# Optimization experiments

Hardware: AMD Instinct MI355X
Metric: run time of the kernel (lower is better)

The kernel has to match this reference:

```python
import jax, jax.numpy as jnp
import numpy as np

B, N, P, K, D = 8, 2048, 64, 32, 384
DEPTH, DI, DS, DCONV, DTR, NC = 12, 768, 16, 4, 24, 40
BN_EPS = 1e-5


def _spread_bits(v):
    v = v & 1023
    v = (v | (v << 16)) & 50331903
    v = (v | (v << 8)) & 50393103
    v = (v | (v << 4)) & 51130563
    v = (v | (v << 2)) & 153391689
    return v


def _zkey(x, y, z):
    return _spread_bits(x) | (_spread_bits(y) << 1) | (_spread_bits(z) << 2)


def _sfc_order(xyz, trans):
    lo = xyz.min(0, keepdims=True)
    hi = xyz.max(0, keepdims=True)
    q = jnp.clip(((xyz - lo) / (hi - lo + 1e-6) * 1023.0).astype(jnp.int32), 0, 1023)
    if trans:
        keys = _zkey(q[:, 2], q[:, 1], q[:, 0])
    else:
        keys = _zkey(q[:, 0], q[:, 1], q[:, 2])
    return jnp.argsort(keys)


def _ln(x, g, b):
    m = x.mean(-1, keepdims=True)
    v = jnp.var(x, axis=-1, keepdims=True)
    return (x - m) / jnp.sqrt(v + 1e-5) * g + b


def _bn_eval(x, g, b):
    # BatchNorm in eval mode, running_mean=0 / running_var=1
    return x * (g / np.float32(np.sqrt(1.0 + BN_EPS))) + b


def _patch_embed_one(xyz, w1, b1, g1, be1, w2, b2, g2, be2, w3, b3, g3, be3):
    # xyz: (N,3)
    cidx = (jnp.arange(P) * (N / P)).astype(jnp.int32)
    centers = xyz[cidx]                                      # (P,3)
    d2 = ((centers[:, None, :] - xyz[None, :, :]) ** 2).sum(-1)  # (P,N)
    _, knn = jax.lax.top_k(-d2, K)                           # (P,K) smallest dists
    nx = xyz[knn] - centers[:, None, :]                      # (P,K,3)
    h = jax.nn.gelu(_bn_eval(nx @ w1.T + b1, g1, be1), approximate=False)   # (P,K,64)
    h = jax.nn.gelu(_bn_eval(h @ w2.T + b2, g2, be2), approximate=False)    # (P,K,128)
    h = _bn_eval(h @ w3.T + b3, g3, be3)                     # (P,K,384)
    return h.max(1), centers


def _mamba(x, in_w, conv_w, conv_b, xp_w, dt_w, dt_b, Alog, Dp, out_w):
    # x: (B,L,D)
    Bsz, L, _ = x.shape
    xz = x @ in_w.T                                          # (B,L,2*DI)
    xc, z = xz[..., :DI], xz[..., DI:]
    xpad = jnp.pad(xc, ((0, 0), (DCONV - 1, 0), (0, 0)))
    xc = sum(xpad[:, j:j + L, :] * conv_w[:, j] for j in range(DCONV)) + conv_b
    xc = jax.nn.silu(xc)
    x_dbl = xc @ xp_w.T                                      # (B,L,DTR+2*DS)
    dt = x_dbl[..., :DTR]
    Bm = x_dbl[..., DTR:DTR + DS]
    Cm = x_dbl[..., DTR + DS:]
    delta = jax.nn.softplus(dt @ dt_w.T + dt_b)              # (B,L,DI)
    A = -jnp.exp(Alog)                                       # (DI,DS)

    def step(h, inp):
        d_t, B_t, C_t, u_t = inp                             # (B,DI),(B,DS),(B,DS),(B,DI)
        h = h * jnp.exp(d_t[..., None] * A) + (d_t * u_t)[..., None] * B_t[:, None, :]
        return h, jnp.einsum('bds,bs->bd', h, C_t)

    h0 = jnp.zeros((Bsz, DI, DS), x.dtype)
    inps = (delta.transpose(1, 0, 2), Bm.transpose(1, 0, 2),
            Cm.transpose(1, 0, 2), xc.transpose(1, 0, 2))
    _, ys = jax.lax.scan(step, h0, inps)                     # (L,B,DI)
    y = ys.transpose(1, 0, 2) + Dp * xc
    y = y * jax.nn.silu(z)
    return y @ out_w.T


def setup_inputs() -> dict:
    key = jax.random.key(0)
    ks = iter(jax.random.split(key, 64))
    nrm = lambda *s: jax.random.normal(next(ks), s, jnp.float32) * 0.02
    inp = {
        'data': jax.random.normal(next(ks), (B, N, 3), jnp.float32),
        'pe_w1': nrm(64, 3), 'pe_b1': jnp.zeros(64), 'pe_g1': jnp.ones(64), 'pe_be1': jnp.zeros(64),
        'pe_w2': nrm(128, 64), 'pe_b2': jnp.zeros(128), 'pe_g2': jnp.ones(128), 'pe_be2': jnp.zeros(128),
        'pe_w3': nrm(D, 128), 'pe_b3': jnp.zeros(D), 'pe_g3': jnp.ones(D), 'pe_be3': jnp.zeros(D),
        'oi_h_scale': jnp.ones(D), 'oi_h_shift': jnp.zeros(D),
        'oi_th_scale': jnp.ones(D), 'oi_th_shift': jnp.zeros(D),
        'pos_embed': nrm(1, P, D),
        'blk_ln_g': jnp.ones((DEPTH, D)), 'blk_ln_b': jnp.zeros((DEPTH, D)),
        'blk_in_w': nrm(DEPTH, 2 * DI, D),
        'blk_conv_w': nrm(DEPTH, DI, DCONV), 'blk_conv_b': jnp.zeros((DEPTH, DI)),
        'blk_xp_w': nrm(DEPTH, DTR + 2 * DS, DI),
        'blk_dt_w': nrm(DEPTH, DI, DTR), 'blk_dt_b': jnp.full((DEPTH, DI), -4.0),
        'blk_Alog': jnp.tile(jnp.log(jnp.arange(1, DS + 1, dtype=jnp.float32)), (DEPTH, DI, 1)),
        'blk_D': jnp.ones((DEPTH, DI)),
        'blk_out_w': nrm(DEPTH, D, DI),
        'norm_g': jnp.ones(D), 'norm_b': jnp.zeros(D),
        'mlp_w1': nrm(256, D), 'mlp_b1': jnp.zeros(256),
        'mlp_w2': nrm(64, 256), 'mlp_b2': jnp.zeros(64),
        'mlp_w3': nrm(NC, 64), 'mlp_b3': jnp.zeros(NC),
    }
    return inp


def reference(data, pe_w1, pe_b1, pe_g1, pe_be1, pe_w2, pe_b2, pe_g2, pe_be2,
              pe_w3, pe_b3, pe_g3, pe_be3, oi_h_scale, oi_h_shift, oi_th_scale,
              oi_th_shift, pos_embed, blk_ln_g, blk_ln_b, blk_in_w, blk_conv_w,
              blk_conv_b, blk_xp_w, blk_dt_w, blk_dt_b, blk_Alog, blk_D,
              blk_out_w, norm_g, norm_b, mlp_w1, mlp_b1, mlp_w2, mlp_b2,
              mlp_w3, mlp_b3):
    xyz = data[:, :, :3]
    tokens, centers = jax.vmap(
        _patch_embed_one, in_axes=(0,) + (None,) * 12)(
        xyz, pe_w1, pe_b1, pe_g1, pe_be1, pe_w2, pe_b2, pe_g2, pe_be2,
        pe_w3, pe_b3, pe_g3, pe_be3)                         # (B,P,D),(B,P,3)
    order_h = jax.vmap(lambda c: _sfc_order(c, False))(centers)
    order_th = jax.vmap(lambda c: _sfc_order(c, True))(centers)
    th = jnp.take_along_axis(tokens, order_h[:, :, None], axis=1) * oi_h_scale + oi_h_shift
    tth = jnp.take_along_axis(tokens, order_th[:, :, None], axis=1) * oi_th_scale + oi_th_shift
    t = jnp.concatenate([th + pos_embed, tth + pos_embed], axis=1)  # (B,2P,D)
    for i in range(DEPTH):
        t = t + _mamba(_ln(t, blk_ln_g[i], blk_ln_b[i]),
                       blk_in_w[i], blk_conv_w[i], blk_conv_b[i], blk_xp_w[i],
                       blk_dt_w[i], blk_dt_b[i], blk_Alog[i], blk_D[i], blk_out_w[i])
    t = _ln(t, norm_g, norm_b)
    x = t.mean(1)
    x = jax.nn.relu(x @ mlp_w1.T + mlp_b1)
    x = jax.nn.relu(x @ mlp_w2.T + mlp_b2)
    return x @ mlp_w3.T + mlp_b3
```

## Files before the change

kernel.cpp:

```cpp
#include <hip/hip_runtime.h>
#include <math.h>

#define BB 8
#define NN 2048
#define PP 64
#define KK 32
#define DD 384
#define DEPTH 12
#define DI 768
#define DS 16
#define DCONV 4
#define DTR 24
#define NC 40
#define LL 128
#define XROW (DTR + 2 * DS)
#define NR (BB * LL)
#define XPARTS 12

using bf16x8 = __attribute__((ext_vector_type(8))) short;
using floatx4 = __attribute__((ext_vector_type(4))) float;

__device__ __forceinline__ float gelu_exact(float x) {
    return 0.5f * x * (1.0f + erff(x * 0.70710678118654752440f));
}
__device__ __forceinline__ float siluf(float x) {
    return x / (1.0f + expf(-x));
}
__device__ __forceinline__ unsigned short f2bf(float f) {
    unsigned u = __float_as_uint(f);
    u += 0x7fffu + ((u >> 16) & 1u);
    return (unsigned short)(u >> 16);
}
__device__ __forceinline__ float bf2f(short s) {
    return __uint_as_float(((unsigned)(unsigned short)s) << 16);
}
__device__ __forceinline__ unsigned spread_bits(unsigned v) {
    v &= 1023u;
    v = (v | (v << 16)) & 50331903u;
    v = (v | (v << 8)) & 50393103u;
    v = (v | (v << 4)) & 51130563u;
    v = (v | (v << 2)) & 153391689u;
    return v;
}

__global__ void k_cvt(const float* __restrict__ in_w, const float* __restrict__ out_w,
                      const float* __restrict__ pe_w3, const float* __restrict__ xp,
                      unsigned short* __restrict__ inwbf, unsigned short* __restrict__ owbf,
                      unsigned short* __restrict__ w3bf, unsigned short* __restrict__ xpbf)
{
    int idx = blockIdx.x * 256 + threadIdx.x;
    const int n1 = DEPTH * 2 * DI * DD;
    const int n2 = DEPTH * DD * DI;
    const int n3 = DD * 128;
    const int n4 = DEPTH * 64 * DI;
    if (idx < n1) { inwbf[idx] = f2bf(in_w[idx]); return; }
    idx -= n1;
    if (idx < n2) { owbf[idx] = f2bf(out_w[idx]); return; }
    idx -= n2;
    if (idx < n3) { w3bf[idx] = f2bf(pe_w3[idx]); return; }
    idx -= n3;
    if (idx < n4) {
        int i = idx / (64 * DI);
        int rem = idx - i * 64 * DI;
        int n = rem / DI, k = rem % DI;
        float v = (n < XROW) ? xp[(size_t)i * XROW * DI + (size_t)n * DI + k] : 0.f;
        xpbf[idx] = f2bf(v);
    }
}

__global__ __launch_bounds__(256) void k_knn(const float* __restrict__ data,
                                             int* __restrict__ knn_out,
                                             float* __restrict__ centers)
{
    const int bp = blockIdx.x;
    const int b = bp >> 6, p = bp & 63;
    const int tid = threadIdx.x;
    const int lane = tid & 63, wid = tid >> 6;
    const float* X = data + (size_t)b * NN * 3;

    const float cx = X[p * 32 * 3 + 0];
    const float cy = X[p * 32 * 3 + 1];
    const float cz = X[p * 32 * 3 + 2];
    if (tid == 0) {
        centers[(b * PP + p) * 3 + 0] = cx;
        centers[(b * PP + p) * 3 + 1] = cy;
        centers[(b * PP + p) * 3 + 2] = cz;
    }

    unsigned long long pk[8];
#pragma unroll
    for (int q = 0; q < 8; q++) {
        int i = tid + 256 * q;
        float dx = cx - X[i * 3 + 0];
        float dy = cy - X[i * 3 + 1];
        float dz = cz - X[i * 3 + 2];
        float d2 = dx * dx + dy * dy + dz * dz;
        pk[q] = ((unsigned long long)__float_as_uint(d2) << 32) | (unsigned)i;
    }

    __shared__ unsigned long long wred[4];
    __shared__ int klist[KK];
    for (int k = 0; k < KK; k++) {
        unsigned long long m = pk[0];
#pragma unroll
        for (int q = 1; q < 8; q++) m = pk[q] < m ? pk[q] : m;
#pragma unroll
        for (int off = 32; off; off >>= 1) {
            unsigned long long o = __shfl_xor(m, off);
            m = o < m ? o : m;
        }
        if (lane == 0) wred[wid] = m;
        __syncthreads();
        unsigned long long g = wred[0];
#pragma unroll
        for (int w = 1; w < 4; w++) g = wred[w] < g ? wred[w] : g;
#pragma unroll
        for (int q = 0; q < 8; q++)
            if (pk[q] == g) pk[q] = ~0ull;
        if (tid == 0) klist[k] = (int)(g & 0xffffffffu);
        __syncthreads();
    }
    if (tid < KK) knn_out[bp * KK + tid] = klist[tid];
}

__global__ __launch_bounds__(256) void k_pe_mlp(
    const float* __restrict__ data, const int* __restrict__ knn_in,
    const float* __restrict__ w1, const float* __restrict__ b1,
    const float* __restrict__ g1, const float* __restrict__ be1,
    const float* __restrict__ w2, const float* __restrict__ b2,
    const float* __restrict__ g2, const float* __restrict__ be2,
    const unsigned short* __restrict__ w3bf, const float* __restrict__ b3,
    const float* __restrict__ g3, const float* __restrict__ be3,
    float* __restrict__ tokens)
{
    const int bp = blockIdx.x;
    const int b = bp >> 6, p = bp & 63;
    const int tid = threadIdx.x;
    const float* X = data + (size_t)b * NN * 3;
    const float inv_den = 0.99999500003749968752f;

    __shared__ float nxs[KK * 3];
    __shared__ float h1s[KK * 64];
    __shared__ short h2b[KK * 136];

    const float cx = X[p * 32 * 3 + 0];
    const float cy = X[p * 32 * 3 + 1];
    const float cz = X[p * 32 * 3 + 2];
    if (tid < KK) {
        int q = knn_in[bp * KK + tid];
        nxs[tid * 3 + 0] = X[q * 3 + 0] - cx;
        nxs[tid * 3 + 1] = X[q * 3 + 1] - cy;
        nxs[tid * 3 + 2] = X[q * 3 + 2] - cz;
    }
    __syncthreads();

    for (int e = tid; e < KK * 64; e += 256) {
        int j = e >> 6, c = e & 63;
        float v = nxs[j * 3 + 0] * w1[c * 3 + 0] + nxs[j * 3 + 1] * w1[c * 3 + 1] +
                  nxs[j * 3 + 2] * w1[c * 3 + 2] + b1[c];
        v = v * (g1[c] * inv_den) + be1[c];
        h1s[j * 64 + c] = gelu_exact(v);
    }
    __syncthreads();

    for (int e = tid; e < KK * 128; e += 256) {
        int j = e >> 7, c = e & 127;
        const float4* wr = (const float4*)(w2 + (size_t)c * 64);
        const float4* hr = (const float4*)(h1s + j * 64);
        float acc = 0.f;
#pragma unroll
        for (int q = 0; q < 16; q++) {
            float4 wv = wr[q], hv = hr[q];
            acc += hv.x * wv.x + hv.y * wv.y + hv.z * wv.z + hv.w * wv.w;
        }
        float v = (acc + b2[c]) * (g2[c] * inv_den) + be2[c];
        h2b[j * 136 + c] = (short)f2bf(gelu_exact(v));
    }
    __syncthreads();

    const int wave = tid >> 6, lane = tid & 63;
    const int quad = lane >> 4, r = lane & 15;
    floatx4 acc3[2][6] = {};
#pragma unroll
    for (int ks = 0; ks < 4; ks++) {
        const int k0 = ks * 32;
        bf16x8 af[2];
        af[0] = *(const bf16x8*)(h2b + (size_t)r * 136 + quad * 8 + k0);
        af[1] = *(const bf16x8*)(h2b + (size_t)(16 + r) * 136 + quad * 8 + k0);
        bf16x8 bfv[6];
#pragma unroll
        for (int nj = 0; nj < 6; nj++) {
            int n = wave * 96 + nj * 16 + r;
            bfv[nj] = *(const bf16x8*)(w3bf + (size_t)n * 128 + quad * 8 + k0);
        }
#pragma unroll
        for (int mi = 0; mi < 2; mi++)
#pragma unroll
            for (int nj = 0; nj < 6; nj++)
                acc3[mi][nj] = __builtin_amdgcn_mfma_f32_16x16x32_bf16(af[mi], bfv[nj], acc3[mi][nj], 0, 0, 0);
    }
#pragma unroll
    for (int nj = 0; nj < 6; nj++) {
        int col = wave * 96 + nj * 16 + r;
        float sc = g3[col] * inv_den;
        float offc = b3[col] * sc + be3[col];
        float m = -3.4e38f;
#pragma unroll
        for (int mi = 0; mi < 2; mi++)
#pragma unroll
            for (int r2 = 0; r2 < 4; r2++)
                m = fmaxf(m, acc3[mi][nj][r2] * sc + offc);
        m = fmaxf(m, __shfl_xor(m, 16));
        m = fmaxf(m, __shfl_xor(m, 32));
        if (quad == 0) tokens[(size_t)bp * DD + col] = m;
    }
}

__global__ __launch_bounds__(64) void k_sfc(const float* __restrict__ centers,
                                            int* __restrict__ order_h,
                                            int* __restrict__ order_th)
{
    const int b = blockIdx.x;
    const int tid = threadIdx.x;
    float cc[3];
    cc[0] = centers[(b * PP + tid) * 3 + 0];
    cc[1] = centers[(b * PP + tid) * 3 + 1];
    cc[2] = centers[(b * PP + tid) * 3 + 2];

    __shared__ float csh[PP][3];
    __shared__ float slo[3], shi[3];
    csh[tid][0] = cc[0]; csh[tid][1] = cc[1]; csh[tid][2] = cc[2];
    __syncthreads();
    if (tid == 0) {
        for (int k = 0; k < 3; k++) {
            float lo = csh[0][k], hi = csh[0][k];
            for (int j = 1; j < PP; j++) { lo = fminf(lo, csh[j][k]); hi = fmaxf(hi, csh[j][k]); }
            slo[k] = lo; shi[k] = hi;
        }
    }
    __syncthreads();

    int q[3];
    for (int k = 0; k < 3; k++) {
        float t = (cc[k] - slo[k]) / (shi[k] - slo[k] + 1e-6f) * 1023.0f;
        int qi = (int)t;
        qi = qi < 0 ? 0 : (qi > 1023 ? 1023 : qi);
        q[k] = qi;
    }
    unsigned kh = spread_bits((unsigned)q[0]) | (spread_bits((unsigned)q[1]) << 1) |
                  (spread_bits((unsigned)q[2]) << 2);
    unsigned kt = spread_bits((unsigned)q[2]) | (spread_bits((unsigned)q[1]) << 1) |
                  (spread_bits((unsigned)q[0]) << 2);

    __shared__ unsigned khs[PP], kts[PP];
    khs[tid] = kh; kts[tid] = kt;
    __syncthreads();
    int rh = 0, rt = 0;
    for (int j = 0; j < PP; j++) {
        unsigned a = khs[j];
        rh += (a < kh) || (a == kh && j < tid);
        unsigned c = kts[j];
        rt += (c < kt) || (c == kt && j < tid);
    }
    order_h[b * PP + rh] = tid;
    order_th[b * PP + rt] = tid;
}

__global__ void k_build_t(const float* __restrict__ tokens,
                          const int* __restrict__ order_h, const int* __restrict__ order_th,
                          const float* __restrict__ hs, const float* __restrict__ hb,
                          const float* __restrict__ ts, const float* __restrict__ tb,
                          const float* __restrict__ pos, float* __restrict__ t)
{
    int idx = blockIdx.x * blockDim.x + threadIdx.x;
    if (idx >= BB * LL * DD) return;
    int d = idx % DD;
    int l = (idx / DD) % LL;
    int b = idx / (DD * LL);
    float v;
    if (l < PP) {
        int src = order_h[b * PP + l];
        v = tokens[((size_t)b * PP + src) * DD + d] * hs[d] + hb[d] + pos[l * DD + d];
    } else {
        int ll2 = l - PP;
        int src = order_th[b * PP + ll2];
        v = tokens[((size_t)b * PP + src) * DD + d] * ts[d] + tb[d] + pos[ll2 * DD + d];
    }
    t[idx] = v;
}

__global__ __launch_bounds__(256) void k_stats(const float* __restrict__ t,
                                               const float* __restrict__ g,
                                               const float* __restrict__ gb,
                                               unsigned short* __restrict__ tbf)
{
    const int tid = threadIdx.x;
    const int wid = tid >> 6, lane = tid & 63;
    const int row = blockIdx.x * 4 + wid;
    const size_t base = (size_t)row * DD;
    float v[6];
    float s = 0.f, q = 0.f;
#pragma unroll
    for (int j = 0; j < 6; j++) {
        v[j] = t[base + lane + 64 * j];
        s += v[j]; q += v[j] * v[j];
    }
#pragma unroll
    for (int off = 32; off; off >>= 1) { s += __shfl_xor(s, off); q += __shfl_xor(q, off); }
    float mean = s * (1.0f / DD);
    float var = q * (1.0f / DD) - mean * mean;
    float inv = 1.0f / sqrtf(var + 1e-5f);
#pragma unroll
    for (int j = 0; j < 6; j++) {
        int i = lane + 64 * j;
        tbf[base + i] = f2bf((v[j] - mean) * inv * g[i] + gb[i]);
    }
}

__global__ __launch_bounds__(256) void k_mfma_xz(
    const unsigned short* __restrict__ tbf,
    const unsigned short* __restrict__ inwbf,
    const float* __restrict__ cw, const float* __restrict__ cb,
    const unsigned short* __restrict__ xpbf,
    unsigned short* __restrict__ xcbf, unsigned short* __restrict__ zsbf,
    float* __restrict__ parts_x)
{
    __shared__ short ct[128][72];
    const int tid = threadIdx.x;
    const int wave = tid >> 6, lane = tid & 63;
    const int quad = lane >> 4, r = lane & 15;
    const int wm = wave >> 1, wn = wave & 1;
    const int b = blockIdx.y;
    const int n0 = blockIdx.x * 64;
    const int m0 = b * 128 + wm * 64;

    floatx4 acc[4][2] = {};
    const unsigned short* Ab = tbf + (size_t)(m0 + r) * DD + quad * 8;
    const unsigned short* Bb = inwbf + (size_t)(n0 + wn * 32 + r) * DD + quad * 8;
    for (int k0 = 0; k0 < DD; k0 += 32) {
        bf16x8 af[4], bfv[2];
#pragma unroll
        for (int i = 0; i < 4; i++)
            af[i] = *(const bf16x8*)(Ab + (size_t)(i * 16) * DD + k0);
#pragma unroll
        for (int j = 0; j < 2; j++)
            bfv[j] = *(const bf16x8*)(Bb + (size_t)(j * 16) * DD + k0);
#pragma unroll
        for (int i = 0; i < 4; i++)
#pragma unroll
            for (int j = 0; j < 2; j++)
                acc[i][j] = __builtin_amdgcn_mfma_f32_16x16x32_bf16(af[i], bfv[j], acc[i][j], 0, 0, 0);
    }

#pragma unroll
    for (int i = 0; i < 4; i++)
#pragma unroll
        for (int r2 = 0; r2 < 4; r2++) {
            short* cp = &ct[wm * 64 + i * 16 + quad * 4 + r2][wn * 32 + r];
#pragma unroll
            for (int j = 0; j < 2; j++)
                cp[j * 16] = (short)f2bf(acc[i][j][r2]);
        }
    __syncthreads();

    const int l0 = (tid >> 3) * 4;
    const int c0 = (tid & 7) * 8;
    if (n0 < DI) {
        float cwv[8][4], cbv[8];
#pragma unroll
        for (int q = 0; q < 8; q++) {
            *(float4*)cwv[q] = *(const float4*)(cw + (size_t)(n0 + c0 + q) * 4);
            cbv[q] = cb[n0 + c0 + q];
        }
        unsigned short ov[4][8];
#pragma unroll
        for (int dl = 0; dl < 4; dl++) {
            const int l = l0 + dl;
            float u[8];
#pragma unroll
            for (int q = 0; q < 8; q++) u[q] = cbv[q];
#pragma unroll
            for (int j = 0; j < DCONV; j++) {
                int lt = l - (DCONV - 1) + j;
                if (lt >= 0) {
                    bf16x8 x = *(const bf16x8*)&ct[lt][c0];
#pragma unroll
                    for (int q = 0; q < 8; q++) u[q] += bf2f(x[q]) * cwv[q][j];
                }
            }
#pragma unroll
            for (int q = 0; q < 8; q++) ov[dl][q] = f2bf(siluf(u[q]));
        }
        __syncthreads();
#pragma unroll
        for (int dl = 0; dl < 4; dl++) {
            const int l = l0 + dl;
            *(bf16x8*)&ct[l][c0] = *(bf16x8*)ov[dl];
            *(bf16x8*)(xcbf + (size_t)(b * LL + l) * DI + n0 + c0) = *(bf16x8*)ov[dl];
        }
        __syncthreads();

        const int zi = blockIdx.x;
        floatx4 acc2[2][4] = {};
#pragma unroll
        for (int k0 = 0; k0 < 64; k0 += 32) {
            bf16x8 af2[2], bfv2[4];
#pragma unroll
            for (int i = 0; i < 2; i++)
                af2[i] = *(const bf16x8*)&ct[wave * 32 + i * 16 + r][k0 + quad * 8];
#pragma unroll
            for (int nj = 0; nj < 4; nj++)
                bfv2[nj] = *(const bf16x8*)(xpbf + (size_t)(nj * 16 + r) * DI + n0 + k0 + quad * 8);
#pragma unroll
            for (int i = 0; i < 2; i++)
#pragma unroll
                for (int nj = 0; nj < 4; nj++)
                    acc2[i][nj] = __builtin_amdgcn_mfma_f32_16x16x32_bf16(af2[i], bfv2[nj], acc2[i][nj], 0, 0, 0);
        }
        float* out = parts_x + (size_t)zi * NR * XROW;
#pragma unroll
        for (int i = 0; i < 2; i++)
#pragma unroll
            for (int nj = 0; nj < 4; nj++) {
                int col = nj * 16 + r;
                if (col < XROW) {
#pragma unroll
                    for (int r2 = 0; r2 < 4; r2++) {
                        int row = b * LL + wave * 32 + i * 16 + quad * 4 + r2;
                        out[(size_t)row * XROW + col] = acc2[i][nj][r2];
                    }
                }
            }
    } else {
        const int nz = n0 - DI;
#pragma unroll
        for (int dl = 0; dl < 4; dl++) {
            const int l = l0 + dl;
            bf16x8 x = *(const bf16x8*)&ct[l][c0];
            unsigned short o[8];
#pragma unroll
            for (int q = 0; q < 8; q++) o[q] = f2bf(siluf(bf2f(x[q])));
            *(bf16x8*)(zsbf + (size_t)(b * LL + l) * DI + nz + c0) = *(bf16x8*)o;
        }
    }
}

__global__ void k_xred(const float* __restrict__ parts, float* __restrict__ xdbl)
{
    int i = blockIdx.x * 256 + threadIdx.x;
    if (i >= NR * XROW) return;
    float s = 0.f;
#pragma unroll
    for (int z = 0; z < XPARTS; z++) s += parts[(size_t)z * NR * XROW + i];
    xdbl[i] = s;
}

__global__ __launch_bounds__(128) void k_scan(
    const float* __restrict__ xdbl,
    const unsigned short* __restrict__ xcbf, const unsigned short* __restrict__ zsbf,
    const float* __restrict__ dtw, const float* __restrict__ dtb,
    const float* __restrict__ Alog, const float* __restrict__ Dp,
    unsigned short* __restrict__ ybf)
{
    const int tid = threadIdx.x;
    const int b = blockIdx.x / DI;
    const int d = blockIdx.x % DI;

    __shared__ float da[LL][17];
    __shared__ float Bsh[LL][17];
    __shared__ float Csh[LL][17];
    __shared__ float dus[LL];
    __shared__ float us[LL];
    __shared__ float zs[LL];
    __shared__ float ApL[DS][9];
    __shared__ float HlL[DS][9];
    __shared__ float hst[DS][9];

    {
        const int t = tid;
        const size_t row = (size_t)b * LL + t;
        const float* xd = xdbl + row * XROW;
        const float* w = dtw + d * DTR;
        float acc = dtb[d];
#pragma unroll
        for (int k = 0; k < DTR; k++) acc += xd[k] * w[k];
        float delta = fmaxf(acc, 0.f) + log1pf(__expf(-fabsf(acc)));
        float u = bf2f((short)xcbf[row * DI + d]);
        dus[t] = delta * u;
        us[t] = u;
        zs[t] = bf2f((short)zsbf[row * DI + d]);
#pragma unroll
        for (int s = 0; s < DS; s++) {
            da[t][s] = __expf(delta * (-__expf(Alog[d * DS + s])));
            Bsh[t][s] = xd[DTR + s];
            Csh[t][s] = xd[DTR + DS + s];
        }
    }
    __syncthreads();

    const int s = tid & 15;
    const int c = tid >> 4;

    {
        float h = 0.f, Ap = 1.f;
#pragma unroll
        for (int q = 0; q < 16; q++) {
            int t = c * 16 + q;
            float a = da[t][s];
            h = h * a + dus[t] * Bsh[t][s];
            Ap *= a;
        }
        ApL[s][c] = Ap;
        HlL[s][c] = h;
    }
    __syncthreads();
    if (tid < DS) {
        float hs = 0.f;
#pragma unroll
        for (int cc = 0; cc < 8; cc++) {
            hst[tid][cc] = hs;
            hs = ApL[tid][cc] * hs + HlL[tid][cc];
        }
    }
    __syncthreads();

    {
        const float Dd = Dp[d];
        float h = hst[s][c];
        unsigned short* yc = ybf + ((size_t)b * LL + c * 16) * DI + d;
#pragma unroll
        for (int q = 0; q < 16; q++) {
            int t = c * 16 + q;
            float a = da[t][s];
            h = h * a + dus[t] * Bsh[t][s];
            float p = h * Csh[t][s];
            p += __shfl_xor(p, 1, 16);
            p += __shfl_xor(p, 2, 16);
            p += __shfl_xor(p, 4, 16);
            p += __shfl_xor(p, 8, 16);
            if (s == 0) yc[(size_t)q * DI] = f2bf((p + Dd * us[t]) * zs[t]);
        }
    }
}

__global__ __launch_bounds__(256) void k_mfma_op(
    const unsigned short* __restrict__ ybf,
    const unsigned short* __restrict__ owbf,
    float* __restrict__ t)
{
    const int tid = threadIdx.x;
    const int wave = tid >> 6, lane = tid & 63;
    const int quad = lane >> 4, r = lane & 15;
    const int wr2 = wave >> 1, wc = wave & 1;
    const int n0 = blockIdx.x * 64 + wc * 32;
    const int m0 = blockIdx.y * 32 + wr2 * 16;

    floatx4 acc[2] = {};
    const unsigned short* Ab = ybf + (size_t)(m0 + r) * DI + quad * 8;
    const unsigned short* Bb = owbf + (size_t)(n0 + r) * DI + quad * 8;
    for (int k0 = 0; k0 < DI; k0 += 32) {
        bf16x8 af = *(const bf16x8*)(Ab + k0);
        bf16x8 b0 = *(const bf16x8*)(Bb + k0);
        bf16x8 b1 = *(const bf16x8*)(Bb + (size_t)16 * DI + k0);
        acc[0] = __builtin_amdgcn_mfma_f32_16x16x32_bf16(af, b0, acc[0], 0, 0, 0);
        acc[1] = __builtin_amdgcn_mfma_f32_16x16x32_bf16(af, b1, acc[1], 0, 0, 0);
    }

#pragma unroll
    for (int j = 0; j < 2; j++) {
        int col = n0 + j * 16 + r;
#pragma unroll
        for (int r2 = 0; r2 < 4; r2++) {
            int row = m0 + quad * 4 + r2;
            float* tp = t + (size_t)row * DD + col;
            *tp += acc[j][r2];
        }
    }
}

__global__ __launch_bounds__(256) void k_lnpool(const float* __restrict__ t,
                                                const float* __restrict__ ng,
                                                const float* __restrict__ nb,
                                                float* __restrict__ pparts)
{
    const int b = blockIdx.y, chunk = blockIdx.x;
    const int tid = threadIdx.x;
    const int wave = tid >> 6, lane = tid & 63;
    __shared__ float pw[4][DD];

    for (int c = lane; c < DD; c += 64) pw[wave][c] = 0.f;
    __syncthreads();

    for (int rr = 0; rr < 4; rr++) {
        const int row = b * LL + chunk * 16 + wave * 4 + rr;
        const float* xr = t + (size_t)row * DD;
        float v[6];
        float s = 0.f, q = 0.f;
#pragma unroll
        for (int j = 0; j < 6; j++) { v[j] = xr[lane + 64 * j]; s += v[j]; q += v[j] * v[j]; }
#pragma unroll
        for (int off = 32; off; off >>= 1) { s += __shfl_xor(s, off); q += __shfl_xor(q, off); }
        float mean = s * (1.0f / DD);
        float var = q * (1.0f / DD) - mean * mean;
        float inv = 1.0f / sqrtf(var + 1e-5f);
#pragma unroll
        for (int j = 0; j < 6; j++) {
            int c = lane + 64 * j;
            pw[wave][c] += (v[j] - mean) * inv * ng[c] + nb[c];
        }
    }
    __syncthreads();
    float* out = pparts + ((size_t)b * 8 + chunk) * DD;
    for (int c = tid; c < DD; c += 256)
        out[c] = pw[0][c] + pw[1][c] + pw[2][c] + pw[3][c];
}

__global__ __launch_bounds__(256) void k_mlp(const float* __restrict__ pparts,
    const float* __restrict__ w1, const float* __restrict__ b1,
    const float* __restrict__ w2, const float* __restrict__ b2,
    const float* __restrict__ w3, const float* __restrict__ b3,
    float* __restrict__ out)
{
    const int b = blockIdx.x, tid = threadIdx.x;
    __shared__ float pl[DD];
    __shared__ float h1[256];
    __shared__ float h2[64];
    for (int c = tid; c < DD; c += 256) {
        const float* pp = pparts + (size_t)b * 8 * DD + c;
        float s = 0.f;
#pragma unroll
        for (int z = 0; z < 8; z++) s += pp[z * DD];
        pl[c] = s * (1.0f / LL);
    }
    __syncthreads();

    {
        float acc = b1[tid];
        const float* wr = w1 + (size_t)tid * DD;
        for (int k = 0; k < DD; k++) acc += pl[k] * wr[k];
        h1[tid] = fmaxf(acc, 0.f);
    }
    __syncthreads();
    if (tid < 64) {
        float acc = b2[tid];
        const float* wr = w2 + (size_t)tid * 256;
        for (int k = 0; k < 256; k++) acc += h1[k] * wr[k];
        h2[tid] = fmaxf(acc, 0.f);
    }
    __syncthreads();
    if (tid < NC) {
        float acc = b3[tid];
        const float* wr = w3 + (size_t)tid * 64;
        for (int k = 0; k < 64; k++) acc += h2[k] * wr[k];
        out[b * NC + tid] = acc;
    }
}

extern "C" void kernel_launch(void* const* d_in, const int* in_sizes, int n_in,
                              void* d_out, int out_size, void* d_ws, size_t ws_size,
                              hipStream_t stream)
{
    const float* data      = (const float*)d_in[0];
    const float* pe_w1     = (const float*)d_in[1];
    const float* pe_b1     = (const float*)d_in[2];
    const float* pe_g1     = (const float*)d_in[3];
    const float* pe_be1    = (const float*)d_in[4];
    const float* pe_w2     = (const float*)d_in[5];
    const float* pe_b2     = (const float*)d_in[6];
    const float* pe_g2     = (const float*)d_in[7];
    const float* pe_be2    = (const float*)d_in[8];
    const float* pe_w3     = (const float*)d_in[9];
    const float* pe_b3     = (const float*)d_in[10];
    const float* pe_g3     = (const float*)d_in[11];
    const float* pe_be3    = (const float*)d_in[12];
    const float* oi_h_scale  = (const float*)d_in[13];
    const float* oi_h_shift  = (const float*)d_in[14];
    const float* oi_th_scale = (const float*)d_in[15];
    const float* oi_th_shift = (const float*)d_in[16];
    const float* pos_embed = (const float*)d_in[17];
    const float* blk_ln_g  = (const float*)d_in[18];
    const float* blk_ln_b  = (const float*)d_in[19];
    const float* blk_in_w  = (const float*)d_in[20];
    const float* blk_conv_w = (const float*)d_in[21];
    const float* blk_conv_b = (const float*)d_in[22];
    const float* blk_xp_w  = (const float*)d_in[23];
    const float* blk_dt_w  = (const float*)d_in[24];
    const float* blk_dt_b  = (const float*)d_in[25];
    const float* blk_Alog  = (const float*)d_in[26];
    const float* blk_D     = (const float*)d_in[27];
    const float* blk_out_w = (const float*)d_in[28];
    const float* norm_g    = (const float*)d_in[29];
    const float* norm_b    = (const float*)d_in[30];
    const float* mlp_w1    = (const float*)d_in[31];
    const float* mlp_b1    = (const float*)d_in[32];
    const float* mlp_w2    = (const float*)d_in[33];
    const float* mlp_b2    = (const float*)d_in[34];
    const float* mlp_w3    = (const float*)d_in[35];
    const float* mlp_b3    = (const float*)d_in[36];

    float* ws = (float*)d_ws;
    size_t off = 0;
    auto alloc = [&](size_t n) { float* p = ws + off; off += (n + 63) & ~(size_t)63; return p; };
    float* tokens  = alloc((size_t)BB * PP * DD);
    float* centers = alloc((size_t)BB * PP * 3);
    int*   order_h = (int*)alloc((size_t)BB * PP);
    int*   order_th= (int*)alloc((size_t)BB * PP);
    int*   knn_idx = (int*)alloc((size_t)BB * PP * KK);
    float* t    = alloc((size_t)NR * DD);
    float* xdbl = alloc((size_t)NR * XROW);
    float* parts_x = alloc((size_t)XPARTS * NR * XROW);
    float* pparts  = alloc((size_t)BB * 8 * DD);
    unsigned short* tbf   = (unsigned short*)alloc((size_t)NR * DD / 2);
    unsigned short* xcbf  = (unsigned short*)alloc((size_t)NR * DI / 2);
    unsigned short* zsbf  = (unsigned short*)alloc((size_t)NR * DI / 2);
    unsigned short* ybf   = (unsigned short*)alloc((size_t)NR * DI / 2);
    unsigned short* inwbf = (unsigned short*)alloc((size_t)DEPTH * 2 * DI * DD / 2);
    unsigned short* owbf  = (unsigned short*)alloc((size_t)DEPTH * DD * DI / 2);
    unsigned short* xpbf  = (unsigned short*)alloc((size_t)DEPTH * 64 * DI / 2);
    unsigned short* w3bf  = (unsigned short*)alloc((size_t)DD * 128 / 2);

    {
        const int total = DEPTH * 2 * DI * DD + DEPTH * DD * DI + DD * 128 + DEPTH * 64 * DI;
        k_cvt<<<(total + 255) / 256, 256, 0, stream>>>(
            blk_in_w, blk_out_w, pe_w3, blk_xp_w, inwbf, owbf, w3bf, xpbf);
    }

    k_knn<<<BB * PP, 256, 0, stream>>>(data, knn_idx, centers);
    k_pe_mlp<<<BB * PP, 256, 0, stream>>>(data, knn_idx,
        pe_w1, pe_b1, pe_g1, pe_be1, pe_w2, pe_b2, pe_g2, pe_be2,
        w3bf, pe_b3, pe_g3, pe_be3, tokens);
    k_sfc<<<BB, 64, 0, stream>>>(centers, order_h, order_th);
    {
        int nt = BB * LL * DD;
        k_build_t<<<(nt + 255) / 256, 256, 0, stream>>>(tokens, order_h, order_th,
            oi_h_scale, oi_h_shift, oi_th_scale, oi_th_shift, pos_embed, t);
    }

    for (int i = 0; i < DEPTH; i++) {
        const float* ln_g = blk_ln_g + i * DD;
        const float* ln_b = blk_ln_b + i * DD;
        const float* cw   = blk_conv_w + (size_t)i * DI * DCONV;
        const float* cb   = blk_conv_b + (size_t)i * DI;
        const float* dtw  = blk_dt_w + (size_t)i * DI * DTR;
        const float* dtb  = blk_dt_b + (size_t)i * DI;
        const float* Al   = blk_Alog + (size_t)i * DI * DS;
        const float* Dpp  = blk_D + (size_t)i * DI;
        const unsigned short* inw = inwbf + (size_t)i * 2 * DI * DD;
        const unsigned short* ow  = owbf + (size_t)i * DD * DI;
        const unsigned short* xpb = xpbf + (size_t)i * 64 * DI;

        k_stats<<<NR / 4, 256, 0, stream>>>(t, ln_g, ln_b, tbf);
        k_mfma_xz<<<dim3(24, BB), 256, 0, stream>>>(
            tbf, inw, cw, cb, xpb, xcbf, zsbf, parts_x);
        k_xred<<<(NR * XROW + 255) / 256, 256, 0, stream>>>(parts_x, xdbl);
        k_scan<<<BB * DI, 128, 0, stream>>>(xdbl, xcbf, zsbf, dtw, dtb, Al, Dpp, ybf);
        k_mfma_op<<<dim3(DD / 64, NR / 32), 256, 0, stream>>>(ybf, ow, t);
    }

    k_lnpool<<<dim3(8, BB), 256, 0, stream>>>(t, norm_g, norm_b, pparts);
    k_mlp<<<BB, 256, 0, stream>>>(pparts, mlp_w1, mlp_b1, mlp_w2, mlp_b2, mlp_w3, mlp_b3,
                                  (float*)d_out);
}
```

Baseline: 1.055 ms.

## Fuse kNN with patch MLP, SFC with token build, and atomically reduce x_proj

kNN selection moves into the patch-embedding kernel, and SFC ordering merges with token building, which removes launches and global round-trips. The per-layer partial-sum buffer plus its reduction kernel give way to atomic adds into xdbl, which the stats kernel now zeroes. k_cvt is vectorised to four elements per thread. The scan kernel computes decay terms on the fly and keeps per-step values in registers instead of large shared arrays. Atomics make the summation order nondeterministic and add contention, and the register arrays raise register pressure in the scan.

```diff
diff --git a/kernel.cpp b/kernel.cpp
--- a/kernel.cpp
+++ b/kernel.cpp
@@ -15,7 +15,6 @@
 #define LL 128
 #define XROW (DTR + 2 * DS)
 #define NR (BB * LL)
-#define XPARTS 12
 
 using bf16x8 = __attribute__((ext_vector_type(8))) short;
 using floatx4 = __attribute__((ext_vector_type(4))) float;
@@ -48,35 +47,68 @@
                       unsigned short* __restrict__ inwbf, unsigned short* __restrict__ owbf,
                       unsigned short* __restrict__ w3bf, unsigned short* __restrict__ xpbf)
 {
-    int idx = blockIdx.x * 256 + threadIdx.x;
+    int idx = (blockIdx.x * 256 + threadIdx.x) * 4;
     const int n1 = DEPTH * 2 * DI * DD;
     const int n2 = DEPTH * DD * DI;
     const int n3 = DD * 128;
     const int n4 = DEPTH * 64 * DI;
-    if (idx < n1) { inwbf[idx] = f2bf(in_w[idx]); return; }
+    if (idx < n1) {
+        float4 v = *(const float4*)(in_w + idx);
+        ushort4 o; o.x = f2bf(v.x); o.y = f2bf(v.y); o.z = f2bf(v.z); o.w = f2bf(v.w);
+        *(ushort4*)(inwbf + idx) = o;
+        return;
+    }
     idx -= n1;
-    if (idx < n2) { owbf[idx] = f2bf(out_w[idx]); return; }
+    if (idx < n2) {
+        float4 v = *(const float4*)(out_w + idx);
+        ushort4 o; o.x = f2bf(v.x); o.y = f2bf(v.y); o.z = f2bf(v.z); o.w = f2bf(v.w);
+        *(ushort4*)(owbf + idx) = o;
+        return;
+    }
     idx -= n2;
-    if (idx < n3) { w3bf[idx] = f2bf(pe_w3[idx]); return; }
+    if (idx < n3) {
+        float4 v = *(const float4*)(pe_w3 + idx);
+        ushort4 o; o.x = f2bf(v.x); o.y = f2bf(v.y); o.z = f2bf(v.z); o.w = f2bf(v.w);
+        *(ushort4*)(w3bf + idx) = o;
+        return;
+    }
     idx -= n3;
     if (idx < n4) {
         int i = idx / (64 * DI);
         int rem = idx - i * 64 * DI;
         int n = rem / DI, k = rem % DI;
-        float v = (n < XROW) ? xp[(size_t)i * XROW * DI + (size_t)n * DI + k] : 0.f;
-        xpbf[idx] = f2bf(v);
-    }
-}
-
-__global__ __launch_bounds__(256) void k_knn(const float* __restrict__ data,
-                                             int* __restrict__ knn_out,
-                                             float* __restrict__ centers)
+        ushort4 o;
+        if (n < XROW) {
+            float4 v = *(const float4*)(xp + (size_t)i * XROW * DI + (size_t)n * DI + k);
+            o.x = f2bf(v.x); o.y = f2bf(v.y); o.z = f2bf(v.z); o.w = f2bf(v.w);
+        } else {
+            o.x = o.y = o.z = o.w = 0;
+        }
+        *(ushort4*)(xpbf + (size_t)i * 64 * DI + (size_t)n * DI + k) = o;
+    }
+}
+
+__global__ __launch_bounds__(256) void k_patch(
+    const float* __restrict__ data,
+    const float* __restrict__ w1, const float* __restrict__ b1,
+    const float* __restrict__ g1, const float* __restrict__ be1,
+    const float* __restrict__ w2, const float* __restrict__ b2,
+    const float* __restrict__ g2, const float* __restrict__ be2,
+    const unsigned short* __restrict__ w3bf, const float* __restrict__ b3,
+    const float* __restrict__ g3, const float* __restrict__ be3,
+    float* __restrict__ tokens, float* __restrict__ centers)
 {
     const int bp = blockIdx.x;
     const int b = bp >> 6, p = bp & 63;
     const int tid = threadIdx.x;
-    const int lane = tid & 63, wid = tid >> 6;
     const float* X = data + (size_t)b * NN * 3;
+    const float inv_den = 0.99999500003749968752f;
+
+    __shared__ unsigned long long wred[4];
+    __shared__ int klist[KK];
+    __shared__ float nxs[KK * 3];
+    __shared__ float h1s[KK * 64];
+    __shared__ short h2b[KK * 136];
 
     const float cx = X[p * 32 * 3 + 0];
     const float cy = X[p * 32 * 3 + 1];
@@ -87,67 +119,42 @@
         centers[(b * PP + p) * 3 + 2] = cz;
     }
 
-    unsigned long long pk[8];
-#pragma unroll
-    for (int q = 0; q < 8; q++) {
-        int i = tid + 256 * q;
-        float dx = cx - X[i * 3 + 0];
-        float dy = cy - X[i * 3 + 1];
-        float dz = cz - X[i * 3 + 2];
-        float d2 = dx * dx + dy * dy + dz * dz;
-        pk[q] = ((unsigned long long)__float_as_uint(d2) << 32) | (unsigned)i;
-    }
-
-    __shared__ unsigned long long wred[4];
-    __shared__ int klist[KK];
-    for (int k = 0; k < KK; k++) {
-        unsigned long long m = pk[0];
-#pragma unroll
-        for (int q = 1; q < 8; q++) m = pk[q] < m ? pk[q] : m;
-#pragma unroll
-        for (int off = 32; off; off >>= 1) {
-            unsigned long long o = __shfl_xor(m, off);
-            m = o < m ? o : m;
-        }
-        if (lane == 0) wred[wid] = m;
-        __syncthreads();
-        unsigned long long g = wred[0];
-#pragma unroll
-        for (int w = 1; w < 4; w++) g = wred[w] < g ? wred[w] : g;
-#pragma unroll
-        for (int q = 0; q < 8; q++)
-            if (pk[q] == g) pk[q] = ~0ull;
-        if (tid == 0) klist[k] = (int)(g & 0xffffffffu);
-        __syncthreads();
-    }
-    if (tid < KK) knn_out[bp * KK + tid] = klist[tid];
-}
-
-__global__ __launch_bounds__(256) void k_pe_mlp(
-    const float* __restrict__ data, const int* __restrict__ knn_in,
-    const float* __restrict__ w1, const float* __restrict__ b1,
-    const float* __restrict__ g1, const float* __restrict__ be1,
-    const float* __restrict__ w2, const float* __restrict__ b2,
-    const float* __restrict__ g2, const float* __restrict__ be2,
-    const unsigned short* __restrict__ w3bf, const float* __restrict__ b3,
-    const float* __restrict__ g3, const float* __restrict__ be3,
-    float* __restrict__ tokens)
-{
-    const int bp = blockIdx.x;
-    const int b = bp >> 6, p = bp & 63;
-    const int tid = threadIdx.x;
-    const float* X = data + (size_t)b * NN * 3;
-    const float inv_den = 0.99999500003749968752f;
-
-    __shared__ float nxs[KK * 3];
-    __shared__ float h1s[KK * 64];
-    __shared__ short h2b[KK * 136];
-
-    const float cx = X[p * 32 * 3 + 0];
-    const float cy = X[p * 32 * 3 + 1];
-    const float cz = X[p * 32 * 3 + 2];
+    {
+        const int lane = tid & 63, wid = tid >> 6;
+        unsigned long long pk[8];
+#pragma unroll
+        for (int q = 0; q < 8; q++) {
+            int i = tid + 256 * q;
+            float dx = cx - X[i * 3 + 0];
+            float dy = cy - X[i * 3 + 1];
+            float dz = cz - X[i * 3 + 2];
+            float d2 = dx * dx + dy * dy + dz * dz;
+            pk[q] = ((unsigned long long)__float_as_uint(d2) << 32) | (unsigned)i;
+        }
+        for (int k = 0; k < KK; k++) {
+            unsigned long long m = pk[0];
+#pragma unroll
+            for (int q = 1; q < 8; q++) m = pk[q] < m ? pk[q] : m;
+#pragma unroll
+            for (int off = 32; off; off >>= 1) {
+                unsigned long long o = __shfl_xor(m, off);
+                m = o < m ? o : m;
+            }
+            if (lane == 0) wred[wid] = m;
+            __syncthreads();
+            unsigned long long g = wred[0];
+#pragma unroll
+            for (int w = 1; w < 4; w++) g = wred[w] < g ? wred[w] : g;
+#pragma unroll
+            for (int q = 0; q < 8; q++)
+                if (pk[q] == g) pk[q] = ~0ull;
+            if (tid == 0) klist[k] = (int)(g & 0xffffffffu);
+            __syncthreads();
+        }
+    }
+
     if (tid < KK) {
-        int q = knn_in[bp * KK + tid];
+        int q = klist[tid];
         nxs[tid * 3 + 0] = X[q * 3 + 0] - cx;
         nxs[tid * 3 + 1] = X[q * 3 + 1] - cy;
         nxs[tid * 3 + 2] = X[q * 3 + 2] - cz;
@@ -216,20 +223,25 @@
     }
 }
 
-__global__ __launch_bounds__(64) void k_sfc(const float* __restrict__ centers,
-                                            int* __restrict__ order_h,
-                                            int* __restrict__ order_th)
-{
-    const int b = blockIdx.x;
+__global__ __launch_bounds__(256) void k_sfc_build(
+    const float* __restrict__ centers, const float* __restrict__ tokens,
+    const float* __restrict__ hs, const float* __restrict__ hb,
+    const float* __restrict__ ts2, const float* __restrict__ tb2,
+    const float* __restrict__ pos, float* __restrict__ tout)
+{
+    const int b = blockIdx.y, part = blockIdx.x;
     const int tid = threadIdx.x;
-    float cc[3];
-    cc[0] = centers[(b * PP + tid) * 3 + 0];
-    cc[1] = centers[(b * PP + tid) * 3 + 1];
-    cc[2] = centers[(b * PP + tid) * 3 + 2];
 
     __shared__ float csh[PP][3];
     __shared__ float slo[3], shi[3];
-    csh[tid][0] = cc[0]; csh[tid][1] = cc[1]; csh[tid][2] = cc[2];
+    __shared__ unsigned khs[PP], kts[PP];
+    __shared__ int oh[PP], ot[PP];
+
+    if (tid < PP) {
+        csh[tid][0] = centers[(b * PP + tid) * 3 + 0];
+        csh[tid][1] = centers[(b * PP + tid) * 3 + 1];
+        csh[tid][2] = centers[(b * PP + tid) * 3 + 2];
+    }
     __syncthreads();
     if (tid == 0) {
         for (int k = 0; k < 3; k++) {
@@ -239,62 +251,63 @@
         }
     }
     __syncthreads();
-
-    int q[3];
-    for (int k = 0; k < 3; k++) {
-        float t = (cc[k] - slo[k]) / (shi[k] - slo[k] + 1e-6f) * 1023.0f;
-        int qi = (int)t;
-        qi = qi < 0 ? 0 : (qi > 1023 ? 1023 : qi);
-        q[k] = qi;
-    }
-    unsigned kh = spread_bits((unsigned)q[0]) | (spread_bits((unsigned)q[1]) << 1) |
-                  (spread_bits((unsigned)q[2]) << 2);
-    unsigned kt = spread_bits((unsigned)q[2]) | (spread_bits((unsigned)q[1]) << 1) |
-                  (spread_bits((unsigned)q[0]) << 2);
-
-    __shared__ unsigned khs[PP], kts[PP];
-    khs[tid] = kh; kts[tid] = kt;
-    __syncthreads();
-    int rh = 0, rt = 0;
-    for (int j = 0; j < PP; j++) {
-        unsigned a = khs[j];
-        rh += (a < kh) || (a == kh && j < tid);
-        unsigned c = kts[j];
-        rt += (c < kt) || (c == kt && j < tid);
-    }
-    order_h[b * PP + rh] = tid;
-    order_th[b * PP + rt] = tid;
-}
-
-__global__ void k_build_t(const float* __restrict__ tokens,
-                          const int* __restrict__ order_h, const int* __restrict__ order_th,
-                          const float* __restrict__ hs, const float* __restrict__ hb,
-                          const float* __restrict__ ts, const float* __restrict__ tb,
-                          const float* __restrict__ pos, float* __restrict__ t)
-{
-    int idx = blockIdx.x * blockDim.x + threadIdx.x;
-    if (idx >= BB * LL * DD) return;
-    int d = idx % DD;
-    int l = (idx / DD) % LL;
-    int b = idx / (DD * LL);
-    float v;
-    if (l < PP) {
-        int src = order_h[b * PP + l];
-        v = tokens[((size_t)b * PP + src) * DD + d] * hs[d] + hb[d] + pos[l * DD + d];
-    } else {
-        int ll2 = l - PP;
-        int src = order_th[b * PP + ll2];
-        v = tokens[((size_t)b * PP + src) * DD + d] * ts[d] + tb[d] + pos[ll2 * DD + d];
-    }
-    t[idx] = v;
+    if (tid < PP) {
+        int q[3];
+        for (int k = 0; k < 3; k++) {
+            float t = (csh[tid][k] - slo[k]) / (shi[k] - slo[k] + 1e-6f) * 1023.0f;
+            int qi = (int)t;
+            qi = qi < 0 ? 0 : (qi > 1023 ? 1023 : qi);
+            q[k] = qi;
+        }
+        khs[tid] = spread_bits((unsigned)q[0]) | (spread_bits((unsigned)q[1]) << 1) |
+                   (spread_bits((unsigned)q[2]) << 2);
+        kts[tid] = spread_bits((unsigned)q[2]) | (spread_bits((unsigned)q[1]) << 1) |
+                   (spread_bits((unsigned)q[0]) << 2);
+    }
+    __syncthreads();
+    if (tid < PP) {
+        unsigned kh = khs[tid], kt = kts[tid];
+        int rh = 0, rt = 0;
+        for (int j = 0; j < PP; j++) {
+            unsigned a = khs[j];
+            rh += (a < kh) || (a == kh && j < tid);
+            unsigned c = kts[j];
+            rt += (c < kt) || (c == kt && j < tid);
+        }
+        oh[rh] = tid;
+        ot[rt] = tid;
+    }
+    __syncthreads();
+
+    const int base = part * (LL * DD / 24);
+    for (int e = tid; e < LL * DD / 24; e += 256) {
+        int idx = base + e;
+        int d = idx % DD;
+        int l = idx / DD;
+        float v;
+        if (l < PP) {
+            int src = oh[l];
+            v = tokens[((size_t)b * PP + src) * DD + d] * hs[d] + hb[d] + pos[l * DD + d];
+        } else {
+            int l2 = l - PP;
+            int src = ot[l2];
+            v = tokens[((size_t)b * PP + src) * DD + d] * ts2[d] + tb2[d] + pos[l2 * DD + d];
+        }
+        tout[(size_t)b * LL * DD + idx] = v;
+    }
 }
 
 __global__ __launch_bounds__(256) void k_stats(const float* __restrict__ t,
                                                const float* __restrict__ g,
                                                const float* __restrict__ gb,
-                                               unsigned short* __restrict__ tbf)
+                                               unsigned short* __restrict__ tbf,
+                                               float* __restrict__ xdbl)
 {
     const int tid = threadIdx.x;
+    {
+        int gi = blockIdx.x * 256 + tid;
+        if (gi < NR * XROW) xdbl[gi] = 0.f;
+    }
     const int wid = tid >> 6, lane = tid & 63;
     const int row = blockIdx.x * 4 + wid;
     const size_t base = (size_t)row * DD;
@@ -323,7 +336,7 @@
     const float* __restrict__ cw, const float* __restrict__ cb,
     const unsigned short* __restrict__ xpbf,
     unsigned short* __restrict__ xcbf, unsigned short* __restrict__ zsbf,
-    float* __restrict__ parts_x)
+    float* __restrict__ xdbl)
 {
     __shared__ short ct[128][72];
     const int tid = threadIdx.x;
@@ -400,7 +413,6 @@
         }
         __syncthreads();
 
-        const int zi = blockIdx.x;
         floatx4 acc2[2][4] = {};
 #pragma unroll
         for (int k0 = 0; k0 < 64; k0 += 32) {
@@ -417,7 +429,6 @@
                 for (int nj = 0; nj < 4; nj++)
                     acc2[i][nj] = __builtin_amdgcn_mfma_f32_16x16x32_bf16(af2[i], bfv2[nj], acc2[i][nj], 0, 0, 0);
         }
-        float* out = parts_x + (size_t)zi * NR * XROW;
 #pragma unroll
         for (int i = 0; i < 2; i++)
 #pragma unroll
@@ -427,7 +438,7 @@
 #pragma unroll
                     for (int r2 = 0; r2 < 4; r2++) {
                         int row = b * LL + wave * 32 + i * 16 + quad * 4 + r2;
-                        out[(size_t)row * XROW + col] = acc2[i][nj][r2];
+                        unsafeAtomicAdd(&xdbl[(size_t)row * XROW + col], acc2[i][nj][r2]);
                     }
                 }
             }
@@ -443,16 +454,6 @@
             *(bf16x8*)(zsbf + (size_t)(b * LL + l) * DI + nz + c0) = *(bf16x8*)o;
         }
     }
-}
-
-__global__ void k_xred(const float* __restrict__ parts, float* __restrict__ xdbl)
-{
-    int i = blockIdx.x * 256 + threadIdx.x;
-    if (i >= NR * XROW) return;
-    float s = 0.f;
-#pragma unroll
-    for (int z = 0; z < XPARTS; z++) s += parts[(size_t)z * NR * XROW + i];
-    xdbl[i] = s;
 }
 
 __global__ __launch_bounds__(128) void k_scan(
@@ -466,12 +467,11 @@
     const int b = blockIdx.x / DI;
     const int d = blockIdx.x % DI;
 
-    __shared__ float da[LL][17];
-    __shared__ float Bsh[LL][17];
-    __shared__ float Csh[LL][17];
-    __shared__ float dus[LL];
-    __shared__ float us[LL];
-    __shared__ float zs[LL];
+    __shared__ float sdel[LL];
+    __shared__ float sdus[LL];
+    __shared__ float sus[LL];
+    __shared__ float szs[LL];
+    __shared__ float negA[DS];
     __shared__ float ApL[DS][9];
     __shared__ float HlL[DS][9];
     __shared__ float hst[DS][9];
@@ -483,31 +483,39 @@
         const float* w = dtw + d * DTR;
         float acc = dtb[d];
 #pragma unroll
-        for (int k = 0; k < DTR; k++) acc += xd[k] * w[k];
+        for (int k = 0; k < DTR; k += 4) {
+            float4 xv = *(const float4*)(xd + k);
+            float4 wv = *(const float4*)(w + k);
+            acc += xv.x * wv.x + xv.y * wv.y + xv.z * wv.z + xv.w * wv.w;
+        }
         float delta = fmaxf(acc, 0.f) + log1pf(__expf(-fabsf(acc)));
         float u = bf2f((short)xcbf[row * DI + d]);
-        dus[t] = delta * u;
-        us[t] = u;
-        zs[t] = bf2f((short)zsbf[row * DI + d]);
-#pragma unroll
-        for (int s = 0; s < DS; s++) {
-            da[t][s] = __expf(delta * (-__expf(Alog[d * DS + s])));
-            Bsh[t][s] = xd[DTR + s];
-            Csh[t][s] = xd[DTR + DS + s];
-        }
-    }
+        sdel[t] = delta;
+        sdus[t] = delta * u;
+        sus[t] = u;
+        szs[t] = bf2f((short)zsbf[row * DI + d]);
+    }
+    if (tid < DS) negA[tid] = -__expf(Alog[d * DS + tid]);
     __syncthreads();
 
     const int s = tid & 15;
     const int c = tid >> 4;
-
+    const float* xB = xdbl + ((size_t)b * LL + c * 16) * XROW + DTR + s;
+
+    float a_r[16], duB_r[16], C_r[16];
     {
         float h = 0.f, Ap = 1.f;
+        const float na = negA[s];
 #pragma unroll
         for (int q = 0; q < 16; q++) {
             int t = c * 16 + q;
-            float a = da[t][s];
-            h = h * a + dus[t] * Bsh[t][s];
+            float a = __expf(sdel[t] * na);
+            float Bv = xB[(size_t)q * XROW];
+            float Cv = xB[(size_t)q * XROW + DS];
+            a_r[q] = a;
+            duB_r[q] = sdus[t] * Bv;
+            C_r[q] = Cv;
+            h = h * a + duB_r[q];
             Ap *= a;
         }
         ApL[s][c] = Ap;
@@ -530,15 +538,16 @@
         unsigned short* yc = ybf + ((size_t)b * LL + c * 16) * DI + d;
 #pragma unroll
         for (int q = 0; q < 16; q++) {
-            int t = c * 16 + q;
-            float a = da[t][s];
-            h = h * a + dus[t] * Bsh[t][s];
-            float p = h * Csh[t][s];
+            h = h * a_r[q] + duB_r[q];
+            float p = h * C_r[q];
             p += __shfl_xor(p, 1, 16);
             p += __shfl_xor(p, 2, 16);
             p += __shfl_xor(p, 4, 16);
             p += __shfl_xor(p, 8, 16);
-            if (s == 0) yc[(size_t)q * DI] = f2bf((p + Dd * us[t]) * zs[t]);
+            if (s == 0) {
+                int t = c * 16 + q;
+                yc[(size_t)q * DI] = f2bf((p + Dd * sus[t]) * szs[t]);
+            }
         }
     }
 }
@@ -703,12 +712,8 @@
     auto alloc = [&](size_t n) { float* p = ws + off; off += (n + 63) & ~(size_t)63; return p; };
     float* tokens  = alloc((size_t)BB * PP * DD);
     float* centers = alloc((size_t)BB * PP * 3);
-    int*   order_h = (int*)alloc((size_t)BB * PP);
-    int*   order_th= (int*)alloc((size_t)BB * PP);
-    int*   knn_idx = (int*)alloc((size_t)BB * PP * KK);
     float* t    = alloc((size_t)NR * DD);
     float* xdbl = alloc((size_t)NR * XROW);
-    float* parts_x = alloc((size_t)XPARTS * NR * XROW);
     float* pparts  = alloc((size_t)BB * 8 * DD);
     unsigned short* tbf   = (unsigned short*)alloc((size_t)NR * DD / 2);
     unsigned short* xcbf  = (unsigned short*)alloc((size_t)NR * DI / 2);
@@ -721,20 +726,15 @@
 
     {
         const int total = DEPTH * 2 * DI * DD + DEPTH * DD * DI + DD * 128 + DEPTH * 64 * DI;
-        k_cvt<<<(total + 255) / 256, 256, 0, stream>>>(
+        k_cvt<<<(total / 4 + 255) / 256, 256, 0, stream>>>(
             blk_in_w, blk_out_w, pe_w3, blk_xp_w, inwbf, owbf, w3bf, xpbf);
     }
 
-    k_knn<<<BB * PP, 256, 0, stream>>>(data, knn_idx, centers);
-    k_pe_mlp<<<BB * PP, 256, 0, stream>>>(data, knn_idx,
+    k_patch<<<BB * PP, 256, 0, stream>>>(data,
         pe_w1, pe_b1, pe_g1, pe_be1, pe_w2, pe_b2, pe_g2, pe_be2,
-        w3bf, pe_b3, pe_g3, pe_be3, tokens);
-    k_sfc<<<BB, 64, 0, stream>>>(centers, order_h, order_th);
-    {
-        int nt = BB * LL * DD;
-        k_build_t<<<(nt + 255) / 256, 256, 0, stream>>>(tokens, order_h, order_th,
-            oi_h_scale, oi_h_shift, oi_th_scale, oi_th_shift, pos_embed, t);
-    }
+        w3bf, pe_b3, pe_g3, pe_be3, tokens, centers);
+    k_sfc_build<<<dim3(24, BB), 256, 0, stream>>>(centers, tokens,
+        oi_h_scale, oi_h_shift, oi_th_scale, oi_th_shift, pos_embed, t);
 
     for (int i = 0; i < DEPTH; i++) {
         const float* ln_g = blk_ln_g + i * DD;
@@ -749,10 +749,9 @@
         const unsigned short* ow  = owbf + (size_t)i * DD * DI;
         const unsigned short* xpb = xpbf + (size_t)i * 64 * DI;
 
-        k_stats<<<NR / 4, 256, 0, stream>>>(t, ln_g, ln_b, tbf);
+        k_stats<<<NR / 4, 256, 0, stream>>>(t, ln_g, ln_b, tbf, xdbl);
         k_mfma_xz<<<dim3(24, BB), 256, 0, stream>>>(
-            tbf, inw, cw, cb, xpb, xcbf, zsbf, parts_x);
-        k_xred<<<(NR * XROW + 255) / 256, 256, 0, stream>>>(parts_x, xdbl);
+            tbf, inw, cw, cb, xpb, xcbf, zsbf, xdbl);
         k_scan<<<BB * DI, 128, 0, stream>>>(xdbl, xcbf, zsbf, dtw, dtb, Al, Dpp, ybf);
         k_mfma_op<<<dim3(DD / 64, NR / 32), 256, 0, stream>>>(ybf, ow, t);
     }
```

Result: faster. 960.6 us (-9.0%).
